# Kernel optimization log

Measured on AMD Instinct MI355X. Metric: run time of the kernel, lower is better.

Reference implementation:

```python
import jax, jax.numpy as jnp
import numpy as np

TEMPERATURE = 0.1
NUM_RISK_GROUPS = 4
SIM_WEIGHT = 1.0
CONTRAST_WEIGHT = 0.1
NEG = jnp.float32(-1e9)  # finite stand-in for -inf (grad-safe, exp() == 0 in fp32)


def setup_inputs() -> dict:
    key = jax.random.key(0)
    k1, k2, k3, k4 = jax.random.split(key, 4)
    N, D = 8192, 256
    return {
        "log_risks": jax.random.normal(k1, (N,), dtype=jnp.float32),
        "times": jax.random.uniform(k2, (N,), dtype=jnp.float32),
        "censor": jnp.ones((N,), dtype=jnp.int32),
        "wsi_embeddings": jax.random.normal(k3, (N, D), dtype=jnp.float32),
        "omic_embeddings": jax.random.normal(k4, (N, D), dtype=jnp.float32),
    }


def _cox_loss(log_risks, times, censor):
    lr = jnp.clip(log_risks, -10.0, 10.0)
    order = jnp.argsort(-times)  # descending times
    slr = lr[order]
    sc = censor[order]
    # at-risk sum for index i is sum_{j<=i} exp(slr_j) (arange <= i mask) -> cumsum
    at_risk = jnp.cumsum(jnp.exp(slr))
    li = slr - jnp.log(at_risk + 1e-15)
    mask = (sc == 1)
    cnt = jnp.maximum(jnp.sum(mask), 1)
    return -jnp.sum(jnp.where(mask, li, 0.0)) / cnt


def _similarity_loss(a, b):
    na = jnp.maximum(jnp.linalg.norm(a, axis=1), 1e-8)
    nb = jnp.maximum(jnp.linalg.norm(b, axis=1), 1e-8)
    cos = jnp.clip(jnp.sum(a * b, axis=1) / (na * nb), -1.0, 1.0)
    return jnp.mean(1.0 - cos)


def _contrastive_loss(emb, times):
    # NOTE: assumes censor == 1 for all samples (as in setup_inputs), so the
    # uncensored subset is the whole batch and shapes stay static.
    G = NUM_RISK_GROUPS
    q = jnp.quantile(times, jnp.linspace(0.0, 1.0, G + 1))
    # group = #thresholds q[1..G] that t >= ; max bucket clipped to G-1
    groups = jnp.clip(jnp.sum(times[:, None] >= q[None, 1:], axis=1), 0, G - 1)
    z = emb / jnp.maximum(jnp.linalg.norm(emb, axis=1, keepdims=True), 1e-12)
    sim = (z @ z.T) / TEMPERATURE  # [N, N]
    N = emb.shape[0]
    eye = jnp.eye(N, dtype=bool)
    same = groups[:, None] == groups[None, :]
    pos = same & ~eye
    offdiag = ~eye  # pos | neg == all off-diagonal entries
    lse_pos = jax.nn.logsumexp(jnp.where(pos, sim, NEG), axis=1)
    lse_all = jax.nn.logsumexp(jnp.where(offdiag, sim, NEG), axis=1)
    neg_any = jnp.any(~same & ~eye, axis=1)
    valid = jnp.any(pos, axis=1) & neg_any
    loss = -lse_pos + lse_all
    cnt = jnp.maximum(jnp.sum(valid), 1)
    return jnp.sum(jnp.where(valid, loss, 0.0)) / cnt


def reference(log_risks, times, censor, wsi_embeddings, omic_embeddings):
    cox = _cox_loss(log_risks, times, censor)
    sim = _similarity_loss(wsi_embeddings, omic_embeddings)
    c_wsi = _contrastive_loss(wsi_embeddings, times)
    c_omic = _contrastive_loss(omic_embeddings, times)
    contrast = (c_wsi + c_omic) / 2.0
    return cox + SIM_WEIGHT * sim + CONTRAST_WEIGHT * contrast
```

## Files before the change

### kernel.cpp

```cpp
#include <hip/hip_runtime.h>


#define NN 8192
#define DD 256

typedef __attribute__((ext_vector_type(4))) float f32x4;
typedef __attribute__((ext_vector_type(4))) int i32x4;
typedef __attribute__((ext_vector_type(8))) int i32x8;

__global__ void __launch_bounds__(256) k_rows(
    const float* __restrict__ lr, const float* __restrict__ times,
    const int* __restrict__ censor,
    const float* __restrict__ wsi, const float* __restrict__ omic,
    unsigned char* __restrict__ pw, unsigned char* __restrict__ po,
    float* __restrict__ pslots, float* __restrict__ gsum) {
  __shared__ __align__(16) float st[1024];
  __shared__ __align__(16) float se[1024];
  __shared__ float red[4][3];
  const int tid = threadIdx.x;
  const int lane = tid & 63;
  const int wv = tid >> 6;
  const int i = blockIdx.x * 4 + wv;

  if (blockIdx.x < 64) {
    ((f32x4*)gsum)[blockIdx.x * 256 + tid] = (f32x4){0.f, 0.f, 0.f, 0.f};
  }

  const float4 w = ((const float4*)(wsi + (size_t)i * DD))[lane];
  const float4 o = ((const float4*)(omic + (size_t)i * DD))[lane];
  float nw = w.x * w.x + w.y * w.y + w.z * w.z + w.w * w.w;
  float no = o.x * o.x + o.y * o.y + o.z * o.z + o.w * o.w;
  float dd = w.x * o.x + w.y * o.y + w.z * o.z + w.w * o.w;
  for (int m = 1; m < 64; m <<= 1) {
    nw += __shfl_xor(nw, m);
    no += __shfl_xor(no, m);
    dd += __shfl_xor(dd, m);
  }
  const float nws = sqrtf(nw), nos = sqrtf(no);

  const float ti = times[i];
  int rk = 0;
  float ar = 0.f;
  for (int c = 0; c < 8; ++c) {
    __syncthreads();
    for (int p = tid; p < 1024; p += 256) {
      float t = times[c * 1024 + p];
      float l = lr[c * 1024 + p];
      st[p] = t;
      se[p] = __expf(fminf(fmaxf(l, -10.f), 10.f));
    }
    __syncthreads();
#pragma unroll 4
    for (int jt = 0; jt < 16; ++jt) {
      const int p = jt * 64 + lane;
      const float t = st[p];
      const float e = se[p];
      const bool c1 = (t < ti) || ((t == ti) && ((c * 1024 + p) < i));
      rk += c1 ? 1 : 0;
      ar += c1 ? 0.f : e;
    }
  }
  for (int m = 1; m < 64; m <<= 1) {
    rk += __shfl_xor(rk, m);
    ar += __shfl_xor(ar, m);
  }

  if (lane == 0) {
    float c = dd / (fmaxf(nws, 1e-8f) * fmaxf(nos, 1e-8f));
    c = fminf(fmaxf(c, -1.f), 1.f);
    float l = fminf(fmaxf(lr[i], -10.f), 10.f);
    float li = l - logf(ar + 1e-15f);
    bool cen = (censor[i] == 1);
    red[wv][0] = cen ? li : 0.f;
    red[wv][1] = cen ? 1.f : 0.f;
    red[wv][2] = 1.f - c;
  }

  const int r = rk;
  const float iw = 1.f / fmaxf(nws, 1e-12f);
  const float io = 1.f / fmaxf(nos, 1e-12f);
  int zw = __builtin_amdgcn_cvt_pk_fp8_f32(w.x * iw, w.y * iw, 0, false);
  zw = __builtin_amdgcn_cvt_pk_fp8_f32(w.z * iw, w.w * iw, zw, true);
  int zo = __builtin_amdgcn_cvt_pk_fp8_f32(o.x * io, o.y * io, 0, false);
  zo = __builtin_amdgcn_cvt_pk_fp8_f32(o.z * io, o.w * io, zo, true);
  const size_t off = ((size_t)((lane >> 5) * 4 + ((lane >> 3) & 3)) * NN + r) * 32
                     + (lane & 7) * 4;
  *(unsigned int*)(pw + off) = (unsigned int)zw;
  *(unsigned int*)(po + off) = (unsigned int)zo;
  __syncthreads();
  if (tid < 3) {
    pslots[blockIdx.x * 4 + tid] =
        red[0][tid] + red[1][tid] + red[2][tid] + red[3][tid];
  }
}

__device__ inline void epi(const f32x4& a0, const f32x4& a1, int t,
                           int dt0, int dt1, int lo, int q,
                           float* __restrict__ s0, float* __restrict__ s1) {
  if (t == dt0 || t == dt1) {
#pragma unroll
    for (int r = 0; r < 4; ++r) {
      float e0 = __builtin_amdgcn_exp2f(fmaf(a0[r], 14.4269504f, -14.4269504f));
      float e1 = __builtin_amdgcn_exp2f(fmaf(a1[r], 14.4269504f, -14.4269504f));
      if (t == dt0 && lo == q * 4 + r) e0 = 0.f;
      if (t == dt1 && lo == q * 4 + r) e1 = 0.f;
      s0[r] += e0;
      s1[r] += e1;
    }
  } else {
#pragma unroll
    for (int r = 0; r < 4; ++r) {
      s0[r] += __builtin_amdgcn_exp2f(fmaf(a0[r], 14.4269504f, -14.4269504f));
      s1[r] += __builtin_amdgcn_exp2f(fmaf(a1[r], 14.4269504f, -14.4269504f));
    }
  }
}

__global__ void __launch_bounds__(256, 4) k_contrast(
    const unsigned char* __restrict__ pw, const unsigned char* __restrict__ po,
    float* __restrict__ gsum) {
  const int tid = threadIdx.x;
  const int lane = tid & 63;
  const int wv = tid >> 6;
  const int lo = lane & 15, q = lane >> 4;
  const int cb = blockIdx.x, rb = blockIdx.y, mz = blockIdx.z;
  const unsigned char* __restrict__ pk = (mz == 0) ? pw : po;
  const int rowbase = rb * 128 + wv * 32;
  const int colstart = cb * 512;
  const int g = cb >> 2;

  i32x8 afrag[2][2];
#pragma unroll
  for (int rt = 0; rt < 2; ++rt) {
    const size_t row = rowbase + rt * 16 + lo;
#pragma unroll
    for (int ks = 0; ks < 2; ++ks)
      afrag[rt][ks] = *(const i32x8*)(pk + ((size_t)(ks * 4 + q) * NN + row) * 32);
  }

  const unsigned char* const bbase0 =
      pk + ((size_t)q * NN + colstart + lo) * 32;
  const unsigned char* const bbase1 =
      pk + ((size_t)(4 + q) * NN + colstart + lo) * 32;

  const int dt0 = (rowbase - colstart) >> 4;
  const int dt1 = dt0 + 1;

  float s0[4] = {0.f, 0.f, 0.f, 0.f};
  float s1[4] = {0.f, 0.f, 0.f, 0.f};
  f32x4 acc0[2], acc1[2];
  i32x8 bcur[2], bnxt[2];
  bcur[0] = *(const i32x8*)bbase0;
  bcur[1] = *(const i32x8*)bbase1;

#pragma unroll 2
  for (int t = 0; t < 32; ++t) {
    const int cur = t & 1, oth = cur ^ 1;
    if (t < 31) {
      bnxt[0] = *(const i32x8*)(bbase0 + (size_t)(t + 1) * 512);
      bnxt[1] = *(const i32x8*)(bbase1 + (size_t)(t + 1) * 512);
    }
    f32x4 z = {0.f, 0.f, 0.f, 0.f};
    acc0[cur] = z; acc1[cur] = z;
    acc0[cur] = __builtin_amdgcn_mfma_scale_f32_16x16x128_f8f6f4(
        afrag[0][0], bcur[0], acc0[cur], 0, 0, 0, 0x7F, 0, 0x7F);
    acc1[cur] = __builtin_amdgcn_mfma_scale_f32_16x16x128_f8f6f4(
        afrag[1][0], bcur[0], acc1[cur], 0, 0, 0, 0x7F, 0, 0x7F);
    acc0[cur] = __builtin_amdgcn_mfma_scale_f32_16x16x128_f8f6f4(
        afrag[0][1], bcur[1], acc0[cur], 0, 0, 0, 0x7F, 0, 0x7F);
    acc1[cur] = __builtin_amdgcn_mfma_scale_f32_16x16x128_f8f6f4(
        afrag[1][1], bcur[1], acc1[cur], 0, 0, 0, 0x7F, 0, 0x7F);
    if (t > 0) epi(acc0[oth], acc1[oth], t - 1, dt0, dt1, lo, q, s0, s1);
    bcur[0] = bnxt[0];
    bcur[1] = bnxt[1];
  }
  epi(acc0[1], acc1[1], 31, dt0, dt1, lo, q, s0, s1);

#pragma unroll
  for (int rt = 0; rt < 2; ++rt)
#pragma unroll
    for (int r = 0; r < 4; ++r) {
      float v = rt ? s1[r] : s0[r];
      v += __shfl_xor(v, 1); v += __shfl_xor(v, 2);
      v += __shfl_xor(v, 4); v += __shfl_xor(v, 8);
      if (lo == 0) {
        const int row = rowbase + rt * 16 + q * 4 + r;
        atomicAdd(&gsum[((size_t)mz * NN + row) * 4 + g], v);
      }
    }
}

__global__ void __launch_bounds__(1024) k_finale(
    const float* __restrict__ pslots, const float* __restrict__ gsum,
    float* __restrict__ out) {
  __shared__ float rsum[16][4];
  const int tid = threadIdx.x;
  const int lane = tid & 63, wv = tid >> 6;
  float cox = 0.f, cnt = 0.f, sim = 0.f, con = 0.f;
  for (int b = tid; b < 2048; b += 1024) {
    const float4 v = ((const float4*)pslots)[b];
    cox += v.x; cnt += v.y; sim += v.z;
  }
  for (int idx = tid; idx < 2 * NN; idx += 1024) {
    const float4 v = ((const float4*)gsum)[idx];
    const int row = idx & (NN - 1);
    const int gg = row >> 11;
    const float sg = (gg == 0) ? v.x : (gg == 1) ? v.y : (gg == 2) ? v.z : v.w;
    con += logf(v.x + v.y + v.z + v.w) - logf(sg);
  }
  for (int m = 1; m < 64; m <<= 1) {
    cox += __shfl_xor(cox, m);
    cnt += __shfl_xor(cnt, m);
    sim += __shfl_xor(sim, m);
    con += __shfl_xor(con, m);
  }
  if (lane == 0) {
    rsum[wv][0] = cox; rsum[wv][1] = cnt; rsum[wv][2] = sim; rsum[wv][3] = con;
  }
  __syncthreads();
  if (tid == 0) {
    float c0 = 0.f, c1 = 0.f, c2 = 0.f, c3 = 0.f;
    for (int k = 0; k < 16; ++k) {
      c0 += rsum[k][0]; c1 += rsum[k][1]; c2 += rsum[k][2]; c3 += rsum[k][3];
    }
    out[0] = -c0 / fmaxf(c1, 1.f) + c2 / (float)NN
             + 0.1f * 0.5f * c3 / (float)NN;
  }
}

extern "C" void kernel_launch(void* const* d_in, const int* in_sizes, int n_in,
                              void* d_out, int out_size, void* d_ws, size_t ws_size,
                              hipStream_t stream) {
  const float* lr = (const float*)d_in[0];
  const float* times = (const float*)d_in[1];
  const int* censor = (const int*)d_in[2];
  const float* wsi = (const float*)d_in[3];
  const float* omic = (const float*)d_in[4];
  float* out = (float*)d_out;

  char* ws = (char*)d_ws;
  float* pslots = (float*)ws;
  float* gsum = (float*)(ws + 32768);
  unsigned char* pw = (unsigned char*)(ws + 294912);
  unsigned char* po = (unsigned char*)(ws + 294912 + 2097152);

  k_rows<<<2048, 256, 0, stream>>>(lr, times, censor, wsi, omic, pw, po, pslots, gsum);
  k_contrast<<<dim3(16, 64, 2), 256, 0, stream>>>(pw, po, gsum);
  k_finale<<<1, 1024, 0, stream>>>(pslots, gsum, out);
}
```

Measured before the change: 154.9 us.

## Compute exp via MFMA scale bias bit-trick and deepen B prefetch

```diff
diff --git a/kernel.cpp b/kernel.cpp
--- a/kernel.cpp
+++ b/kernel.cpp
@@ -7,6 +7,8 @@
 typedef __attribute__((ext_vector_type(4))) float f32x4;
 typedef __attribute__((ext_vector_type(4))) int i32x4;
 typedef __attribute__((ext_vector_type(8))) int i32x8;
+
+#define ALPHA 3.79828f
 
 __global__ void __launch_bounds__(256) k_rows(
     const float* __restrict__ lr, const float* __restrict__ times,
@@ -77,8 +79,8 @@
   }
 
   const int r = rk;
-  const float iw = 1.f / fmaxf(nws, 1e-12f);
-  const float io = 1.f / fmaxf(nos, 1e-12f);
+  const float iw = ALPHA / fmaxf(nws, 1e-12f);
+  const float io = ALPHA / fmaxf(nos, 1e-12f);
   int zw = __builtin_amdgcn_cvt_pk_fp8_f32(w.x * iw, w.y * iw, 0, false);
   zw = __builtin_amdgcn_cvt_pk_fp8_f32(w.z * iw, w.w * iw, zw, true);
   int zo = __builtin_amdgcn_cvt_pk_fp8_f32(o.x * io, o.y * io, 0, false);
@@ -100,8 +102,8 @@
   if (t == dt0 || t == dt1) {
 #pragma unroll
     for (int r = 0; r < 4; ++r) {
-      float e0 = __builtin_amdgcn_exp2f(fmaf(a0[r], 14.4269504f, -14.4269504f));
-      float e1 = __builtin_amdgcn_exp2f(fmaf(a1[r], 14.4269504f, -14.4269504f));
+      float e0 = __builtin_bit_cast(float, (int)a0[r]);
+      float e1 = __builtin_bit_cast(float, (int)a1[r]);
       if (t == dt0 && lo == q * 4 + r) e0 = 0.f;
       if (t == dt1 && lo == q * 4 + r) e1 = 0.f;
       s0[r] += e0;
@@ -110,8 +112,8 @@
   } else {
 #pragma unroll
     for (int r = 0; r < 4; ++r) {
-      s0[r] += __builtin_amdgcn_exp2f(fmaf(a0[r], 14.4269504f, -14.4269504f));
-      s1[r] += __builtin_amdgcn_exp2f(fmaf(a1[r], 14.4269504f, -14.4269504f));
+      s0[r] += __builtin_bit_cast(float, (int)a0[r]);
+      s1[r] += __builtin_bit_cast(float, (int)a1[r]);
     }
   }
 }
@@ -146,33 +148,35 @@
   const int dt0 = (rowbase - colstart) >> 4;
   const int dt1 = dt0 + 1;
 
+  const float BIAS = (127.0f - 14.4269504f) * 8388608.0f;
+  const f32x4 cinit = {BIAS, BIAS, BIAS, BIAS};
+
   float s0[4] = {0.f, 0.f, 0.f, 0.f};
   float s1[4] = {0.f, 0.f, 0.f, 0.f};
   f32x4 acc0[2], acc1[2];
-  i32x8 bcur[2], bnxt[2];
-  bcur[0] = *(const i32x8*)bbase0;
-  bcur[1] = *(const i32x8*)bbase1;
+  i32x8 bfr[2][2];
+  bfr[0][0] = *(const i32x8*)bbase0;
+  bfr[0][1] = *(const i32x8*)bbase1;
+  bfr[1][0] = *(const i32x8*)(bbase0 + 512);
+  bfr[1][1] = *(const i32x8*)(bbase1 + 512);
 
 #pragma unroll 2
   for (int t = 0; t < 32; ++t) {
     const int cur = t & 1, oth = cur ^ 1;
-    if (t < 31) {
-      bnxt[0] = *(const i32x8*)(bbase0 + (size_t)(t + 1) * 512);
-      bnxt[1] = *(const i32x8*)(bbase1 + (size_t)(t + 1) * 512);
-    }
-    f32x4 z = {0.f, 0.f, 0.f, 0.f};
-    acc0[cur] = z; acc1[cur] = z;
+    acc0[cur] = cinit; acc1[cur] = cinit;
     acc0[cur] = __builtin_amdgcn_mfma_scale_f32_16x16x128_f8f6f4(
-        afrag[0][0], bcur[0], acc0[cur], 0, 0, 0, 0x7F, 0, 0x7F);
+        afrag[0][0], bfr[cur][0], acc0[cur], 0, 0, 0, 0x8B, 0, 0x8A);
     acc1[cur] = __builtin_amdgcn_mfma_scale_f32_16x16x128_f8f6f4(
-        afrag[1][0], bcur[0], acc1[cur], 0, 0, 0, 0x7F, 0, 0x7F);
+        afrag[1][0], bfr[cur][0], acc1[cur], 0, 0, 0, 0x8B, 0, 0x8A);
     acc0[cur] = __builtin_amdgcn_mfma_scale_f32_16x16x128_f8f6f4(
-        afrag[0][1], bcur[1], acc0[cur], 0, 0, 0, 0x7F, 0, 0x7F);
+        afrag[0][1], bfr[cur][1], acc0[cur], 0, 0, 0, 0x8B, 0, 0x8A);
     acc1[cur] = __builtin_amdgcn_mfma_scale_f32_16x16x128_f8f6f4(
-        afrag[1][1], bcur[1], acc1[cur], 0, 0, 0, 0x7F, 0, 0x7F);
+        afrag[1][1], bfr[cur][1], acc1[cur], 0, 0, 0, 0x8B, 0, 0x8A);
+    if (t < 30) {
+      bfr[cur][0] = *(const i32x8*)(bbase0 + (size_t)(t + 2) * 512);
+      bfr[cur][1] = *(const i32x8*)(bbase1 + (size_t)(t + 2) * 512);
+    }
     if (t > 0) epi(acc0[oth], acc1[oth], t - 1, dt0, dt1, lo, q, s0, s1);
-    bcur[0] = bnxt[0];
-    bcur[1] = bnxt[1];
   }
   epi(acc0[1], acc1[1], 31, dt0, dt1, lo, q, s0, s1);
 
```

Measured after the change: 155.3 us. No clear change (+0.3%).
